# Kernel optimization log

Hardware: AMD Instinct MI355X
Metric: run time of the kernel (lower is better)

The kernel has to match this reference:

```python
import jax, jax.numpy as jnp
import numpy as np

HIDDEN = 2048
HEADS = 16
HEAD_DIM = HIDDEN // HEADS
BATCH = 2
SEQ = 2048


def setup_inputs() -> dict:
    key = jax.random.key(0)
    ks = jax.random.split(key, 9)
    s = 0.02
    return {
        "x": jax.random.normal(ks[0], (BATCH, SEQ, HIDDEN), dtype=jnp.float32),
        "Wq": jax.random.normal(ks[1], (HIDDEN, HIDDEN), dtype=jnp.float32) * s,
        "bq": jax.random.normal(ks[2], (HIDDEN,), dtype=jnp.float32) * s,
        "Wk": jax.random.normal(ks[3], (HIDDEN, HIDDEN), dtype=jnp.float32) * s,
        "bk": jax.random.normal(ks[4], (HIDDEN,), dtype=jnp.float32) * s,
        "Wv": jax.random.normal(ks[5], (HIDDEN, HIDDEN), dtype=jnp.float32) * s,
        "bv": jax.random.normal(ks[6], (HIDDEN,), dtype=jnp.float32) * s,
        "Wo": jax.random.normal(ks[7], (HIDDEN, HIDDEN), dtype=jnp.float32) * s,
        "bo": jax.random.normal(ks[8], (HIDDEN,), dtype=jnp.float32) * s,
    }


def reference(x, Wq, bq, Wk, bk, Wv, bv, Wo, bo):
    B, S, H = x.shape
    # Linear layers: y = x @ W.T + b (torch nn.Linear convention, W:[out,in])
    q = x @ Wq.T + bq
    k = x @ Wk.T + bk
    v = x @ Wv.T + bv
    # [B, S, H] -> [B, nH, S, hd]
    def split_heads(t):
        return t.reshape(B, S, HEADS, HEAD_DIM).transpose(0, 2, 1, 3)
    q, k, v = split_heads(q), split_heads(k), split_heads(v)
    scale = 1.0 / (HEAD_DIM ** 0.5)
    # NOTE: original module applies NO causal mask despite its name; be faithful.
    scores = jnp.einsum('bhqd,bhkd->bhqk', q, k) * scale
    probs = jax.nn.softmax(scores, axis=-1)
    attn = jnp.einsum('bhqk,bhkd->bhqd', probs, v)
    attn = attn.transpose(0, 2, 1, 3).reshape(B, S, H)
    return attn @ Wo.T + bo
```

## Files before the change

### kernel.cpp

```cpp
#include <hip/hip_runtime.h>
#include <hip/hip_bf16.h>
#include <stdint.h>

typedef __bf16 bf16_t;
typedef __attribute__((ext_vector_type(8))) __bf16 bf16x8;
typedef __attribute__((ext_vector_type(4))) float floatx4;
typedef __attribute__((ext_vector_type(16))) float f32x16;

typedef __attribute__((address_space(1))) const unsigned int gu32_t;
typedef __attribute__((address_space(3))) unsigned int lu32_t;

__device__ __forceinline__ void async16(const void* g, void* l) {
    __builtin_amdgcn_global_load_lds((gu32_t*)g, (lu32_t*)l, 16, 0, 0);
}

__device__ __forceinline__ uint32_t pack2(float lo, float hi) {
    union { bf16_t h[2]; uint32_t u; } cv;
    cv.h[0] = (bf16_t)lo; cv.h[1] = (bf16_t)hi;
    return cv.u;
}

__global__ __launch_bounds__(256) void cvt_f32_bf16(const float* __restrict__ in,
                                                    bf16_t* __restrict__ out) {
    int i = (blockIdx.x * 256 + threadIdx.x) * 8;
    float4 a = *(const float4*)(in + i);
    float4 b = *(const float4*)(in + i + 4);
    bf16x8 v;
    v[0] = (bf16_t)a.x; v[1] = (bf16_t)a.y; v[2] = (bf16_t)a.z; v[3] = (bf16_t)a.w;
    v[4] = (bf16_t)b.x; v[5] = (bf16_t)b.y; v[6] = (bf16_t)b.z; v[7] = (bf16_t)b.w;
    *(bf16x8*)(out + i) = v;
}

__global__ __launch_bounds__(256) void cvt4_f32_bf16(const float* __restrict__ w0,
                                                     const float* __restrict__ w1,
                                                     const float* __restrict__ w2,
                                                     const float* __restrict__ w3,
                                                     bf16_t* __restrict__ out,
                                                     int elems) {
    const float* srcs[4] = {w0, w1, w2, w3};
    const float* in = srcs[blockIdx.y];
    bf16_t* o = out + (size_t)blockIdx.y * elems;
    int i = (blockIdx.x * 256 + threadIdx.x) * 8;
    float4 a = *(const float4*)(in + i);
    float4 b = *(const float4*)(in + i + 4);
    bf16x8 v;
    v[0] = (bf16_t)a.x; v[1] = (bf16_t)a.y; v[2] = (bf16_t)a.z; v[3] = (bf16_t)a.w;
    v[4] = (bf16_t)b.x; v[5] = (bf16_t)b.y; v[6] = (bf16_t)b.z; v[7] = (bf16_t)b.w;
    *(bf16x8*)(o + i) = v;
}

template <bool OUT_F32, bool BIAS_ROW>
__global__ __launch_bounds__(256) void gemm_bt(const bf16_t* __restrict__ A,
                                               const bf16_t* __restrict__ B,
                                               const float* __restrict__ bias,
                                               const float* __restrict__ bias2,
                                               int nsplit,
                                               float* __restrict__ Cf,
                                               bf16_t* __restrict__ Cb,
                                               int M, int N, int K, int ldc) {
    __shared__ bf16_t As[128 * 64];
    __shared__ bf16_t Bs[128 * 64];
    const int tid = threadIdx.x;
    const int wave = tid >> 6, lane = tid & 63;
    const int quad = lane >> 4, l16 = lane & 15;
    const int wm = (wave >> 1) * 64, wn = (wave & 1) * 64;
    const int tm = blockIdx.x * 128, tn = blockIdx.y * 128;

    floatx4 acc[4][4];
#pragma unroll
    for (int i = 0; i < 4; ++i)
#pragma unroll
        for (int j = 0; j < 4; ++j) acc[i][j] = floatx4{0.f, 0.f, 0.f, 0.f};

    const bf16_t* Abase = A + (size_t)tm * K;
    const bf16_t* Bbase = B + (size_t)tn * K;
    const int sw = l16 & 7;

    for (int kk = 0; kk < K; kk += 64) {
#pragma unroll
        for (int it = 0; it < 4; ++it) {
            int chunk = it * 256 + tid;
            int r = chunk >> 3, c = chunk & 7;
            int c2 = c ^ (r & 7);
            async16(Abase + r * K + kk + c2 * 8, As + (it * 256 + wave * 64) * 8);
            async16(Bbase + r * K + kk + c2 * 8, Bs + (it * 256 + wave * 64) * 8);
        }
        __syncthreads();
#pragma unroll
        for (int ks = 0; ks < 2; ++ks) {
            bf16x8 af[4], bf[4];
#pragma unroll
            for (int mt = 0; mt < 4; ++mt)
                af[mt] = *(const bf16x8*)(As + (wm + mt * 16 + l16) * 64 +
                                          ((ks * 4 + quad) ^ sw) * 8);
#pragma unroll
            for (int nt = 0; nt < 4; ++nt)
                bf[nt] = *(const bf16x8*)(Bs + (wn + nt * 16 + l16) * 64 +
                                          ((ks * 4 + quad) ^ sw) * 8);
#pragma unroll
            for (int mt = 0; mt < 4; ++mt)
#pragma unroll
                for (int nt = 0; nt < 4; ++nt)
                    acc[mt][nt] = __builtin_amdgcn_mfma_f32_16x16x32_bf16(af[mt], bf[nt],
                                                                          acc[mt][nt], 0, 0, 0);
        }
        __syncthreads();
    }
#pragma unroll
    for (int mt = 0; mt < 4; ++mt)
#pragma unroll
        for (int nt = 0; nt < 4; ++nt)
#pragma unroll
            for (int r = 0; r < 4; ++r) {
                int row = tm + wm + mt * 16 + quad * 4 + r;
                int col = tn + wn + nt * 16 + l16;
                float bv = BIAS_ROW ? bias[row]
                                    : (col < nsplit ? bias[col] : bias2[col - nsplit]);
                float v = acc[mt][nt][r] + bv;
                if (OUT_F32) Cf[(size_t)row * ldc + col] = v;
                else Cb[(size_t)row * ldc + col] = (bf16_t)v;
            }
}

#define FA_BUF (64 * 128 + 128 * 64)
__global__ __launch_bounds__(256, 2) void flash_attn(const bf16_t* __restrict__ Qp,
                                                     const bf16_t* __restrict__ Kp,
                                                     const bf16_t* __restrict__ Vt,
                                                     bf16_t* __restrict__ O) {
    __shared__ bf16_t smem[2 * FA_BUF];
    const int tid = threadIdx.x;
    const int wv = tid >> 6, lane = tid & 63;
    const int hi = lane >> 5, l32 = lane & 31;
    const int wq = wv >> 1, wk = wv & 1;
    const int LD = 4096, T = 4096, S = 2048, HO = 2048;
    const float SL2E = 0.088388347688f * 1.44269504089f;

    const int gid = blockIdx.x;
    const int kq = gid >> 3;
    const int qt = kq & 31;
    const int grp = (gid & 7) + 8 * (kq >> 5);
    const int hd = grp & 15, bt = grp >> 4;

    const int qrow0 = bt * S + qt * 64;
    const int krow0 = bt * S;
    const int hoff = hd * 128;
    const int sw7 = l32 & 7;

    const int ck = (4 * 0 * 256 + tid);

    bf16x8 qf[8];
    const bf16_t* qptr = Qp + (size_t)(qrow0 + wq * 32 + l32) * LD + hoff + hi * 8;
#pragma unroll
    for (int ks = 0; ks < 8; ++ks) qf[ks] = *(const bf16x8*)(qptr + ks * 16);

    float l_i = 0.f;
    f32x16 Oacc[4];
#pragma unroll
    for (int dt = 0; dt < 4; ++dt)
#pragma unroll
        for (int r = 0; r < 16; ++r) Oacc[dt][r] = 0.f;

    auto stage = [&](int kt, int b) {
        int kb = krow0 + kt * 64;
        bf16_t* Ks = smem + b * FA_BUF;
        bf16_t* Vts = Ks + 64 * 128;
#pragma unroll
        for (int it = 0; it < 4; ++it) {
            int chunk = it * 256 + tid;
            int r = chunk >> 4, c = chunk & 15;
            int c2 = c ^ (r & 7);
            async16(Kp + (size_t)(kb + r) * LD + hoff + c2 * 8, Ks + chunk * 8);
        }
#pragma unroll
        for (int it = 0; it < 4; ++it) {
            int chunk = it * 256 + tid;
            int r = chunk >> 3, c = chunk & 7;
            int c2 = c ^ (r & 7);
            async16(Vt + (size_t)(hoff + r) * T + kb + c2 * 8, Vts + chunk * 8);
        }
    };

    stage(0, 0);
    for (int kt = 0; kt < 32; ++kt) {
        const int cur = kt & 1;
        __syncthreads();
        if (kt + 1 < 32) stage(kt + 1, cur ^ 1);

        const bf16_t* Ks = smem + cur * FA_BUF;
        const bf16_t* Vts = Ks + 64 * 128;

        f32x16 sf0, sf1;
#pragma unroll
        for (int r = 0; r < 16; ++r) { sf0[r] = 0.f; sf1[r] = 0.f; }
#pragma unroll
        for (int ks = 0; ks < 4; ++ks) {
            bf16x8 a0 = *(const bf16x8*)(Ks + (wk * 32 + l32) * 128 +
                                         ((2 * ks + hi) ^ sw7) * 8);
            bf16x8 a1 = *(const bf16x8*)(Ks + (wk * 32 + l32) * 128 +
                                         ((2 * (ks + 4) + hi) ^ sw7) * 8);
            sf0 = __builtin_amdgcn_mfma_f32_32x32x16_bf16(a0, qf[ks], sf0, 0, 0, 0);
            sf1 = __builtin_amdgcn_mfma_f32_32x32x16_bf16(a1, qf[ks + 4], sf1, 0, 0, 0);
        }

        float rs0 = 0.f, rs1 = 0.f;
        uint32_t pk[8];
#pragma unroll
        for (int a4 = 0; a4 < 4; ++a4) {
            float p0 = exp2f((sf0[4 * a4 + 0] + sf1[4 * a4 + 0]) * SL2E);
            float p1 = exp2f((sf0[4 * a4 + 1] + sf1[4 * a4 + 1]) * SL2E);
            float p2 = exp2f((sf0[4 * a4 + 2] + sf1[4 * a4 + 2]) * SL2E);
            float p3 = exp2f((sf0[4 * a4 + 3] + sf1[4 * a4 + 3]) * SL2E);
            rs0 += p0 + p1;
            rs1 += p2 + p3;
            pk[a4 * 2 + 0] = pack2(p0, p1);
            pk[a4 * 2 + 1] = pack2(p2, p3);
        }
        l_i += rs0 + rs1;

#pragma unroll
        for (int s = 0; s < 2; ++s) {
            uint32_t r0 = (uint32_t)__shfl_xor((int)pk[4 * s + 0], 32);
            uint32_t r1 = (uint32_t)__shfl_xor((int)pk[4 * s + 1], 32);
            uint32_t r2 = (uint32_t)__shfl_xor((int)pk[4 * s + 2], 32);
            uint32_t r3 = (uint32_t)__shfl_xor((int)pk[4 * s + 3], 32);
            union { uint32_t u[4]; bf16x8 v; } w;
            w.u[0] = hi ? r2 : pk[4 * s + 0];
            w.u[1] = hi ? r3 : pk[4 * s + 1];
            w.u[2] = hi ? pk[4 * s + 2] : r0;
            w.u[3] = hi ? pk[4 * s + 3] : r1;
#pragma unroll
            for (int dt = 0; dt < 4; ++dt) {
                bf16x8 a = *(const bf16x8*)(Vts + (dt * 32 + l32) * 64 +
                                            ((4 * wk + 2 * s + hi) ^ sw7) * 8);
                Oacc[dt] = __builtin_amdgcn_mfma_f32_32x32x16_bf16(a, w.v, Oacc[dt], 0, 0, 0);
            }
        }
    }

    __syncthreads();
    l_i += __shfl_xor(l_i, 32);
    float* ml = (float*)smem;
    if (hi == 0) ml[wv * 32 + l32] = l_i;
    __syncthreads();
    float linv = 1.0f / (l_i + ml[(wv ^ 1) * 32 + l32]);
    __syncthreads();

    float* Op = (float*)smem;
    if (wk == 1) {
#pragma unroll
        for (int dt = 0; dt < 4; ++dt)
#pragma unroll
            for (int r = 0; r < 16; ++r) {
                int d = dt * 32 + (r & 3) + 8 * (r >> 2) + 4 * hi;
                Op[(wq * 128 + d) * 32 + l32] = Oacc[dt][r];
            }
    }
    __syncthreads();
    if (wk == 0) {
#pragma unroll
        for (int dt = 0; dt < 4; ++dt)
#pragma unroll
            for (int r = 0; r < 16; ++r) {
                int d = dt * 32 + (r & 3) + 8 * (r >> 2) + 4 * hi;
                Oacc[dt][r] = (Oacc[dt][r] + Op[(wq * 128 + d) * 32 + l32]) * linv;
            }
    }
    __syncthreads();

    if (wk == 0) {
        uint32_t* Os = (uint32_t*)smem + wq * 2048;
#pragma unroll
        for (int dt = 0; dt < 4; ++dt)
#pragma unroll
            for (int a4 = 0; a4 < 4; ++a4) {
                uint32_t q0 = pack2(Oacc[dt][4 * a4 + 0], Oacc[dt][4 * a4 + 1]);
                uint32_t q1 = pack2(Oacc[dt][4 * a4 + 2], Oacc[dt][4 * a4 + 3]);
                int d2 = 16 * dt + 4 * a4 + 2 * hi;
                Os[l32 * 64 + ((d2 + 2 * l32) & 63)] = q0;
                Os[l32 * 64 + ((d2 + 1 + 2 * l32) & 63)] = q1;
            }
#pragma unroll
        for (int r = 0; r < 32; ++r) {
            uint32_t v = Os[r * 64 + ((lane + 2 * r) & 63)];
            uint32_t* orow = (uint32_t*)(O + (size_t)(qrow0 + wq * 32 + r) * HO + hoff);
            orow[lane] = v;
        }
    }
}

extern "C" void kernel_launch(void* const* d_in, const int* in_sizes, int n_in,
                              void* d_out, int out_size, void* d_ws, size_t ws_size,
                              hipStream_t stream) {
    const float* x  = (const float*)d_in[0];
    const float* Wq = (const float*)d_in[1];
    const float* bq = (const float*)d_in[2];
    const float* Wk = (const float*)d_in[3];
    const float* bk = (const float*)d_in[4];
    const float* Wv = (const float*)d_in[5];
    const float* bv = (const float*)d_in[6];
    const float* Wo = (const float*)d_in[7];
    const float* bo = (const float*)d_in[8];
    float* out = (float*)d_out;

    const int T = 4096;
    const int H = 2048;
    bf16_t* ws  = (bf16_t*)d_ws;
    bf16_t* xb  = ws;
    bf16_t* wqb = xb  + (size_t)T * H;
    bf16_t* wkb = wqb + (size_t)H * H;
    bf16_t* wvb = wkb + (size_t)H * H;
    bf16_t* wob = wvb + (size_t)H * H;
    bf16_t* QKb = wob + (size_t)H * H;
    bf16_t* Vtb = QKb + (size_t)T * 2 * H;
    bf16_t* Ab  = Vtb + (size_t)H * T;
    size_t need = (size_t)(Ab + (size_t)T * H - ws) * sizeof(bf16_t);
    if (ws_size < need) return;

    cvt_f32_bf16<<<T * H / 2048, 256, 0, stream>>>(x, xb);
    cvt4_f32_bf16<<<dim3(H * H / 2048, 4), 256, 0, stream>>>(Wq, Wk, Wv, Wo, wqb, H * H);

    dim3 gqk(T / 128, 4096 / 128);
    gemm_bt<false, false><<<gqk, 256, 0, stream>>>(xb, wqb, bq, bk, H,
                                                   nullptr, QKb, T, 4096, H, 4096);
    dim3 gv(H / 128, T / 128);
    gemm_bt<false, true><<<gv, 256, 0, stream>>>(wvb, xb, bv, nullptr, 0,
                                                 nullptr, Vtb, H, T, H, T);

    flash_attn<<<1024, 256, 0, stream>>>(QKb, QKb + H, Vtb, Ab);

    dim3 go(T / 128, H / 128);
    gemm_bt<true, false><<<go, 256, 0, stream>>>(Ab, wob, bo, nullptr, H,
                                                 out, nullptr, T, H, H, H);
}
```

Baseline: 423.9 us.

## Double attention query tile per block and merge conversion and QKV GEMM launches

The flash attention kernel now gives each wave two 32-row query groups, so a block covers 128 query rows. Each K/V tile staged in shared memory is reused across twice as many queries, and the grid is halved. The softmax scale times log2(e) is folded into the Q projection epilogue, which removes a multiply before each exp2 at the cost of rounding the scaled Q to bf16. The separate x and weight conversion kernels are merged into one launch, as are the QK and V projection GEMMs. The larger attention tile roughly doubles accumulator registers per thread, which may lower occupancy or cause spills.

```diff
diff --git a/kernel.cpp b/kernel.cpp
--- a/kernel.cpp
+++ b/kernel.cpp
@@ -10,6 +10,8 @@
 typedef __attribute__((address_space(1))) const unsigned int gu32_t;
 typedef __attribute__((address_space(3))) unsigned int lu32_t;
 
+#define SL2E 0.12753102149f
+
 __device__ __forceinline__ void async16(const void* g, void* l) {
     __builtin_amdgcn_global_load_lds((gu32_t*)g, (lu32_t*)l, 16, 0, 0);
 }
@@ -20,44 +22,116 @@
     return cv.u;
 }
 
-__global__ __launch_bounds__(256) void cvt_f32_bf16(const float* __restrict__ in,
-                                                    bf16_t* __restrict__ out) {
-    int i = (blockIdx.x * 256 + threadIdx.x) * 8;
+__global__ __launch_bounds__(256) void cvt_all(const float* __restrict__ x,
+                                               const float* __restrict__ w0,
+                                               const float* __restrict__ w1,
+                                               const float* __restrict__ w2,
+                                               const float* __restrict__ w3,
+                                               bf16_t* __restrict__ out) {
+    int b = blockIdx.x;
+    const float* in;
+    if (b < 4096) {
+        in = x + (size_t)b * 2048;
+    } else {
+        int t = b - 4096;
+        const float* wsrc[4] = {w0, w1, w2, w3};
+        in = wsrc[t >> 11] + (size_t)(t & 2047) * 2048;
+    }
+    bf16_t* o = out + (size_t)b * 2048;
+    int i = threadIdx.x * 8;
     float4 a = *(const float4*)(in + i);
-    float4 b = *(const float4*)(in + i + 4);
+    float4 c = *(const float4*)(in + i + 4);
     bf16x8 v;
     v[0] = (bf16_t)a.x; v[1] = (bf16_t)a.y; v[2] = (bf16_t)a.z; v[3] = (bf16_t)a.w;
-    v[4] = (bf16_t)b.x; v[5] = (bf16_t)b.y; v[6] = (bf16_t)b.z; v[7] = (bf16_t)b.w;
-    *(bf16x8*)(out + i) = v;
-}
-
-__global__ __launch_bounds__(256) void cvt4_f32_bf16(const float* __restrict__ w0,
-                                                     const float* __restrict__ w1,
-                                                     const float* __restrict__ w2,
-                                                     const float* __restrict__ w3,
-                                                     bf16_t* __restrict__ out,
-                                                     int elems) {
-    const float* srcs[4] = {w0, w1, w2, w3};
-    const float* in = srcs[blockIdx.y];
-    bf16_t* o = out + (size_t)blockIdx.y * elems;
-    int i = (blockIdx.x * 256 + threadIdx.x) * 8;
-    float4 a = *(const float4*)(in + i);
-    float4 b = *(const float4*)(in + i + 4);
-    bf16x8 v;
-    v[0] = (bf16_t)a.x; v[1] = (bf16_t)a.y; v[2] = (bf16_t)a.z; v[3] = (bf16_t)a.w;
-    v[4] = (bf16_t)b.x; v[5] = (bf16_t)b.y; v[6] = (bf16_t)b.z; v[7] = (bf16_t)b.w;
+    v[4] = (bf16_t)c.x; v[5] = (bf16_t)c.y; v[6] = (bf16_t)c.z; v[7] = (bf16_t)c.w;
     *(bf16x8*)(o + i) = v;
 }
 
-template <bool OUT_F32, bool BIAS_ROW>
-__global__ __launch_bounds__(256) void gemm_bt(const bf16_t* __restrict__ A,
-                                               const bf16_t* __restrict__ B,
-                                               const float* __restrict__ bias,
-                                               const float* __restrict__ bias2,
-                                               int nsplit,
-                                               float* __restrict__ Cf,
-                                               bf16_t* __restrict__ Cb,
-                                               int M, int N, int K, int ldc) {
+__global__ __launch_bounds__(256) void gemm_qkv(const bf16_t* __restrict__ xb,
+                                                const bf16_t* __restrict__ wqk,
+                                                const bf16_t* __restrict__ wv,
+                                                const float* __restrict__ bq,
+                                                const float* __restrict__ bk,
+                                                const float* __restrict__ bv,
+                                                bf16_t* __restrict__ QKb,
+                                                bf16_t* __restrict__ Vtb) {
+    __shared__ bf16_t As[128 * 64];
+    __shared__ bf16_t Bs[128 * 64];
+    const int tid = threadIdx.x;
+    const int wave = tid >> 6, lane = tid & 63;
+    const int quad = lane >> 4, l16 = lane & 15;
+    const int wm = (wave >> 1) * 64, wn = (wave & 1) * 64;
+
+    const int bid = blockIdx.x;
+    const bool vmode = bid >= 1024;
+    int tm, tn;
+    const bf16_t *A, *B;
+    bf16_t* Cb;
+    if (!vmode) { tm = (bid & 31) * 128; tn = (bid >> 5) * 128; A = xb; B = wqk; Cb = QKb; }
+    else { int vb = bid - 1024; tm = (vb & 15) * 128; tn = (vb >> 4) * 128; A = wv; B = xb; Cb = Vtb; }
+    const int K = 2048, ldc = 4096;
+
+    floatx4 acc[4][4];
+#pragma unroll
+    for (int i = 0; i < 4; ++i)
+#pragma unroll
+        for (int j = 0; j < 4; ++j) acc[i][j] = floatx4{0.f, 0.f, 0.f, 0.f};
+
+    const bf16_t* Abase = A + (size_t)tm * K;
+    const bf16_t* Bbase = B + (size_t)tn * K;
+    const int sw = l16 & 7;
+
+    for (int kk = 0; kk < K; kk += 64) {
+#pragma unroll
+        for (int it = 0; it < 4; ++it) {
+            int chunk = it * 256 + tid;
+            int r = chunk >> 3, c = chunk & 7;
+            int c2 = c ^ (r & 7);
+            async16(Abase + r * K + kk + c2 * 8, As + (it * 256 + wave * 64) * 8);
+            async16(Bbase + r * K + kk + c2 * 8, Bs + (it * 256 + wave * 64) * 8);
+        }
+        __syncthreads();
+#pragma unroll
+        for (int ks = 0; ks < 2; ++ks) {
+            bf16x8 af[4], bf[4];
+#pragma unroll
+            for (int mt = 0; mt < 4; ++mt)
+                af[mt] = *(const bf16x8*)(As + (wm + mt * 16 + l16) * 64 +
+                                          ((ks * 4 + quad) ^ sw) * 8);
+#pragma unroll
+            for (int nt = 0; nt < 4; ++nt)
+                bf[nt] = *(const bf16x8*)(Bs + (wn + nt * 16 + l16) * 64 +
+                                          ((ks * 4 + quad) ^ sw) * 8);
+#pragma unroll
+            for (int mt = 0; mt < 4; ++mt)
+#pragma unroll
+                for (int nt = 0; nt < 4; ++nt)
+                    acc[mt][nt] = __builtin_amdgcn_mfma_f32_16x16x32_bf16(af[mt], bf[nt],
+                                                                          acc[mt][nt], 0, 0, 0);
+        }
+        __syncthreads();
+    }
+#pragma unroll
+    for (int mt = 0; mt < 4; ++mt)
+#pragma unroll
+        for (int nt = 0; nt < 4; ++nt)
+#pragma unroll
+            for (int r = 0; r < 4; ++r) {
+                int row = tm + wm + mt * 16 + quad * 4 + r;
+                int col = tn + wn + nt * 16 + l16;
+                float v;
+                if (vmode) v = acc[mt][nt][r] + bv[row];
+                else if (col < 2048) v = (acc[mt][nt][r] + bq[col]) * SL2E;
+                else v = acc[mt][nt][r] + bk[col - 2048];
+                Cb[(size_t)row * ldc + col] = (bf16_t)v;
+            }
+}
+
+__global__ __launch_bounds__(256) void gemm_out(const bf16_t* __restrict__ A,
+                                                const bf16_t* __restrict__ B,
+                                                const float* __restrict__ bias,
+                                                float* __restrict__ Cf,
+                                                int K, int ldc) {
     __shared__ bf16_t As[128 * 64];
     __shared__ bf16_t Bs[128 * 64];
     const int tid = threadIdx.x;
@@ -114,11 +188,7 @@
             for (int r = 0; r < 4; ++r) {
                 int row = tm + wm + mt * 16 + quad * 4 + r;
                 int col = tn + wn + nt * 16 + l16;
-                float bv = BIAS_ROW ? bias[row]
-                                    : (col < nsplit ? bias[col] : bias2[col - nsplit]);
-                float v = acc[mt][nt][r] + bv;
-                if (OUT_F32) Cf[(size_t)row * ldc + col] = v;
-                else Cb[(size_t)row * ldc + col] = (bf16_t)v;
+                Cf[(size_t)row * ldc + col] = acc[mt][nt][r] + bias[col];
             }
 }
 
@@ -133,32 +203,34 @@
     const int hi = lane >> 5, l32 = lane & 31;
     const int wq = wv >> 1, wk = wv & 1;
     const int LD = 4096, T = 4096, S = 2048, HO = 2048;
-    const float SL2E = 0.088388347688f * 1.44269504089f;
 
     const int gid = blockIdx.x;
     const int kq = gid >> 3;
-    const int qt = kq & 31;
-    const int grp = (gid & 7) + 8 * (kq >> 5);
+    const int qt = kq & 15;
+    const int grp = (gid & 7) + 8 * (kq >> 4);
     const int hd = grp & 15, bt = grp >> 4;
 
-    const int qrow0 = bt * S + qt * 64;
+    const int qrow0 = bt * S + qt * 128;
     const int krow0 = bt * S;
     const int hoff = hd * 128;
     const int sw7 = l32 & 7;
 
-    const int ck = (4 * 0 * 256 + tid);
-
-    bf16x8 qf[8];
-    const bf16_t* qptr = Qp + (size_t)(qrow0 + wq * 32 + l32) * LD + hoff + hi * 8;
-#pragma unroll
-    for (int ks = 0; ks < 8; ++ks) qf[ks] = *(const bf16x8*)(qptr + ks * 16);
-
-    float l_i = 0.f;
-    f32x16 Oacc[4];
-#pragma unroll
-    for (int dt = 0; dt < 4; ++dt)
-#pragma unroll
-        for (int r = 0; r < 16; ++r) Oacc[dt][r] = 0.f;
+    bf16x8 qf[2][8];
+#pragma unroll
+    for (int g = 0; g < 2; ++g) {
+        const bf16_t* qptr = Qp + (size_t)(qrow0 + wq * 64 + g * 32 + l32) * LD + hoff + hi * 8;
+#pragma unroll
+        for (int ks = 0; ks < 8; ++ks) qf[g][ks] = *(const bf16x8*)(qptr + ks * 16);
+    }
+
+    float l_i[2] = {0.f, 0.f};
+    f32x16 Oacc[2][4];
+#pragma unroll
+    for (int g = 0; g < 2; ++g)
+#pragma unroll
+        for (int dt = 0; dt < 4; ++dt)
+#pragma unroll
+            for (int r = 0; r < 16; ++r) Oacc[g][dt][r] = 0.f;
 
     auto stage = [&](int kt, int b) {
         int kb = krow0 + kt * 64;
@@ -189,102 +261,123 @@
         const bf16_t* Ks = smem + cur * FA_BUF;
         const bf16_t* Vts = Ks + 64 * 128;
 
-        f32x16 sf0, sf1;
-#pragma unroll
-        for (int r = 0; r < 16; ++r) { sf0[r] = 0.f; sf1[r] = 0.f; }
-#pragma unroll
-        for (int ks = 0; ks < 4; ++ks) {
-            bf16x8 a0 = *(const bf16x8*)(Ks + (wk * 32 + l32) * 128 +
-                                         ((2 * ks + hi) ^ sw7) * 8);
-            bf16x8 a1 = *(const bf16x8*)(Ks + (wk * 32 + l32) * 128 +
-                                         ((2 * (ks + 4) + hi) ^ sw7) * 8);
-            sf0 = __builtin_amdgcn_mfma_f32_32x32x16_bf16(a0, qf[ks], sf0, 0, 0, 0);
-            sf1 = __builtin_amdgcn_mfma_f32_32x32x16_bf16(a1, qf[ks + 4], sf1, 0, 0, 0);
-        }
-
-        float rs0 = 0.f, rs1 = 0.f;
-        uint32_t pk[8];
-#pragma unroll
-        for (int a4 = 0; a4 < 4; ++a4) {
-            float p0 = exp2f((sf0[4 * a4 + 0] + sf1[4 * a4 + 0]) * SL2E);
-            float p1 = exp2f((sf0[4 * a4 + 1] + sf1[4 * a4 + 1]) * SL2E);
-            float p2 = exp2f((sf0[4 * a4 + 2] + sf1[4 * a4 + 2]) * SL2E);
-            float p3 = exp2f((sf0[4 * a4 + 3] + sf1[4 * a4 + 3]) * SL2E);
-            rs0 += p0 + p1;
-            rs1 += p2 + p3;
-            pk[a4 * 2 + 0] = pack2(p0, p1);
-            pk[a4 * 2 + 1] = pack2(p2, p3);
-        }
-        l_i += rs0 + rs1;
+        uint32_t pk[2][8];
+#pragma unroll
+        for (int g = 0; g < 2; ++g) {
+            f32x16 sf;
+#pragma unroll
+            for (int r = 0; r < 16; ++r) sf[r] = 0.f;
+#pragma unroll
+            for (int ks = 0; ks < 8; ++ks) {
+                bf16x8 a = *(const bf16x8*)(Ks + (wk * 32 + l32) * 128 +
+                                            ((2 * ks + hi) ^ sw7) * 8);
+                sf = __builtin_amdgcn_mfma_f32_32x32x16_bf16(a, qf[g][ks], sf, 0, 0, 0);
+            }
+            float rs0 = 0.f, rs1 = 0.f;
+#pragma unroll
+            for (int a4 = 0; a4 < 4; ++a4) {
+                float p0 = exp2f(sf[4 * a4 + 0]);
+                float p1 = exp2f(sf[4 * a4 + 1]);
+                float p2 = exp2f(sf[4 * a4 + 2]);
+                float p3 = exp2f(sf[4 * a4 + 3]);
+                rs0 += p0 + p1;
+                rs1 += p2 + p3;
+                pk[g][a4 * 2 + 0] = pack2(p0, p1);
+                pk[g][a4 * 2 + 1] = pack2(p2, p3);
+            }
+            l_i[g] += rs0 + rs1;
+        }
 
 #pragma unroll
         for (int s = 0; s < 2; ++s) {
-            uint32_t r0 = (uint32_t)__shfl_xor((int)pk[4 * s + 0], 32);
-            uint32_t r1 = (uint32_t)__shfl_xor((int)pk[4 * s + 1], 32);
-            uint32_t r2 = (uint32_t)__shfl_xor((int)pk[4 * s + 2], 32);
-            uint32_t r3 = (uint32_t)__shfl_xor((int)pk[4 * s + 3], 32);
-            union { uint32_t u[4]; bf16x8 v; } w;
-            w.u[0] = hi ? r2 : pk[4 * s + 0];
-            w.u[1] = hi ? r3 : pk[4 * s + 1];
-            w.u[2] = hi ? pk[4 * s + 2] : r0;
-            w.u[3] = hi ? pk[4 * s + 3] : r1;
+            union { uint32_t u[4]; bf16x8 v; } w[2];
+#pragma unroll
+            for (int g = 0; g < 2; ++g) {
+                uint32_t r0 = (uint32_t)__shfl_xor((int)pk[g][4 * s + 0], 32);
+                uint32_t r1 = (uint32_t)__shfl_xor((int)pk[g][4 * s + 1], 32);
+                uint32_t r2 = (uint32_t)__shfl_xor((int)pk[g][4 * s + 2], 32);
+                uint32_t r3 = (uint32_t)__shfl_xor((int)pk[g][4 * s + 3], 32);
+                w[g].u[0] = hi ? r2 : pk[g][4 * s + 0];
+                w[g].u[1] = hi ? r3 : pk[g][4 * s + 1];
+                w[g].u[2] = hi ? pk[g][4 * s + 2] : r0;
+                w[g].u[3] = hi ? pk[g][4 * s + 3] : r1;
+            }
 #pragma unroll
             for (int dt = 0; dt < 4; ++dt) {
-                bf16x8 a = *(const bf16x8*)(Vts + (dt * 32 + l32) * 64 +
-                                            ((4 * wk + 2 * s + hi) ^ sw7) * 8);
-                Oacc[dt] = __builtin_amdgcn_mfma_f32_32x32x16_bf16(a, w.v, Oacc[dt], 0, 0, 0);
-            }
-        }
-    }
-
-    __syncthreads();
-    l_i += __shfl_xor(l_i, 32);
+                bf16x8 av = *(const bf16x8*)(Vts + (dt * 32 + l32) * 64 +
+                                             ((4 * wk + 2 * s + hi) ^ sw7) * 8);
+                Oacc[0][dt] = __builtin_amdgcn_mfma_f32_32x32x16_bf16(av, w[0].v, Oacc[0][dt], 0, 0, 0);
+                Oacc[1][dt] = __builtin_amdgcn_mfma_f32_32x32x16_bf16(av, w[1].v, Oacc[1][dt], 0, 0, 0);
+            }
+        }
+    }
+
+    __syncthreads();
     float* ml = (float*)smem;
-    if (hi == 0) ml[wv * 32 + l32] = l_i;
-    __syncthreads();
-    float linv = 1.0f / (l_i + ml[(wv ^ 1) * 32 + l32]);
+#pragma unroll
+    for (int g = 0; g < 2; ++g) l_i[g] += __shfl_xor(l_i[g], 32);
+    if (hi == 0) {
+        ml[(wv * 2 + 0) * 32 + l32] = l_i[0];
+        ml[(wv * 2 + 1) * 32 + l32] = l_i[1];
+    }
+    __syncthreads();
+    float linv[2];
+#pragma unroll
+    for (int g = 0; g < 2; ++g)
+        linv[g] = 1.0f / (l_i[g] + ml[((wv ^ 1) * 2 + g) * 32 + l32]);
     __syncthreads();
 
     float* Op = (float*)smem;
     if (wk == 1) {
 #pragma unroll
-        for (int dt = 0; dt < 4; ++dt)
-#pragma unroll
-            for (int r = 0; r < 16; ++r) {
-                int d = dt * 32 + (r & 3) + 8 * (r >> 2) + 4 * hi;
-                Op[(wq * 128 + d) * 32 + l32] = Oacc[dt][r];
-            }
+        for (int g = 0; g < 2; ++g)
+#pragma unroll
+            for (int dt = 0; dt < 4; ++dt)
+#pragma unroll
+                for (int r = 0; r < 16; ++r) {
+                    int d = dt * 32 + (r & 3) + 8 * (r >> 2) + 4 * hi;
+                    Op[((wq * 2 + g) * 128 + d) * 32 + l32] = Oacc[g][dt][r];
+                }
     }
     __syncthreads();
     if (wk == 0) {
 #pragma unroll
-        for (int dt = 0; dt < 4; ++dt)
-#pragma unroll
-            for (int r = 0; r < 16; ++r) {
-                int d = dt * 32 + (r & 3) + 8 * (r >> 2) + 4 * hi;
-                Oacc[dt][r] = (Oacc[dt][r] + Op[(wq * 128 + d) * 32 + l32]) * linv;
-            }
+        for (int g = 0; g < 2; ++g)
+#pragma unroll
+            for (int dt = 0; dt < 4; ++dt)
+#pragma unroll
+                for (int r = 0; r < 16; ++r) {
+                    int d = dt * 32 + (r & 3) + 8 * (r >> 2) + 4 * hi;
+                    Oacc[g][dt][r] = (Oacc[g][dt][r] +
+                                      Op[((wq * 2 + g) * 128 + d) * 32 + l32]) * linv[g];
+                }
     }
     __syncthreads();
 
     if (wk == 0) {
-        uint32_t* Os = (uint32_t*)smem + wq * 2048;
-#pragma unroll
-        for (int dt = 0; dt < 4; ++dt)
-#pragma unroll
-            for (int a4 = 0; a4 < 4; ++a4) {
-                uint32_t q0 = pack2(Oacc[dt][4 * a4 + 0], Oacc[dt][4 * a4 + 1]);
-                uint32_t q1 = pack2(Oacc[dt][4 * a4 + 2], Oacc[dt][4 * a4 + 3]);
-                int d2 = 16 * dt + 4 * a4 + 2 * hi;
-                Os[l32 * 64 + ((d2 + 2 * l32) & 63)] = q0;
-                Os[l32 * 64 + ((d2 + 1 + 2 * l32) & 63)] = q1;
-            }
-#pragma unroll
-        for (int r = 0; r < 32; ++r) {
-            uint32_t v = Os[r * 64 + ((lane + 2 * r) & 63)];
-            uint32_t* orow = (uint32_t*)(O + (size_t)(qrow0 + wq * 32 + r) * HO + hoff);
-            orow[lane] = v;
-        }
+        uint32_t* Os = (uint32_t*)smem + wq * 4096;
+#pragma unroll
+        for (int g = 0; g < 2; ++g)
+#pragma unroll
+            for (int dt = 0; dt < 4; ++dt)
+#pragma unroll
+                for (int a4 = 0; a4 < 4; ++a4) {
+                    uint32_t q0 = pack2(Oacc[g][dt][4 * a4 + 0], Oacc[g][dt][4 * a4 + 1]);
+                    uint32_t q1 = pack2(Oacc[g][dt][4 * a4 + 2], Oacc[g][dt][4 * a4 + 3]);
+                    int d2 = 16 * dt + 4 * a4 + 2 * hi;
+                    int row = g * 32 + l32;
+                    Os[row * 64 + ((d2 + 2 * l32) & 63)] = q0;
+                    Os[row * 64 + ((d2 + 1 + 2 * l32) & 63)] = q1;
+                }
+    }
+    __syncthreads();
+#pragma unroll
+    for (int r2 = 0; r2 < 32; ++r2) {
+        int rr = wv * 32 + r2;
+        int wqs = rr >> 6, r = rr & 63;
+        uint32_t v = ((uint32_t*)smem)[wqs * 4096 + r * 64 + ((lane + 2 * r) & 63)];
+        uint32_t* orow = (uint32_t*)(O + (size_t)(qrow0 + wqs * 64 + r) * HO + hoff);
+        orow[lane] = v;
     }
 }
 
@@ -307,8 +400,7 @@
     bf16_t* ws  = (bf16_t*)d_ws;
     bf16_t* xb  = ws;
     bf16_t* wqb = xb  + (size_t)T * H;
-    bf16_t* wkb = wqb + (size_t)H * H;
-    bf16_t* wvb = wkb + (size_t)H * H;
+    bf16_t* wvb = wqb + 2 * (size_t)H * H;
     bf16_t* wob = wvb + (size_t)H * H;
     bf16_t* QKb = wob + (size_t)H * H;
     bf16_t* Vtb = QKb + (size_t)T * 2 * H;
@@ -316,19 +408,12 @@
     size_t need = (size_t)(Ab + (size_t)T * H - ws) * sizeof(bf16_t);
     if (ws_size < need) return;
 
-    cvt_f32_bf16<<<T * H / 2048, 256, 0, stream>>>(x, xb);
-    cvt4_f32_bf16<<<dim3(H * H / 2048, 4), 256, 0, stream>>>(Wq, Wk, Wv, Wo, wqb, H * H);
-
-    dim3 gqk(T / 128, 4096 / 128);
-    gemm_bt<false, false><<<gqk, 256, 0, stream>>>(xb, wqb, bq, bk, H,
-                                                   nullptr, QKb, T, 4096, H, 4096);
-    dim3 gv(H / 128, T / 128);
-    gemm_bt<false, true><<<gv, 256, 0, stream>>>(wvb, xb, bv, nullptr, 0,
-                                                 nullptr, Vtb, H, T, H, T);
-
-    flash_attn<<<1024, 256, 0, stream>>>(QKb, QKb + H, Vtb, Ab);
+    cvt_all<<<12288, 256, 0, stream>>>(x, Wq, Wk, Wv, Wo, ws);
+
+    gemm_qkv<<<1536, 256, 0, stream>>>(xb, wqb, wvb, bq, bk, bv, QKb, Vtb);
+
+    flash_attn<<<512, 256, 0, stream>>>(QKb, QKb + H, Vtb, Ab);
 
     dim3 go(T / 128, H / 128);
-    gemm_bt<true, false><<<go, 256, 0, stream>>>(Ab, wob, bo, nullptr, H,
-                                                 out, nullptr, T, H, H, H);
-}
+    gemm_out<<<go, 256, 0, stream>>>(Ab, wob, bo, out, H, H);
+}
```

Result: slower. 456.7 us (+7.7%).
